# Optimization experiments

Measured on AMD Instinct MI355X. Metric: run time of the kernel, lower is better.

Reference implementation:

```python
import jax, jax.numpy as jnp
import numpy as np

B, L, T, F, H, O = 4096, 50, 64, 3, 20, 16

def setup_inputs() -> dict:
    key = jax.random.key(0)
    ks = jax.random.split(key, 20)
    p = lambda k, s: jax.random.normal(k, s, jnp.float32) * 0.1
    inp = {
        'x': jax.random.normal(ks[0], (B, L, T, F), jnp.float32),
        'lengths': jax.random.randint(ks[1], (B, L), 0, T, jnp.int32),
        # LSTMCell params (torch gate order i,f,g,o)
        'w_ih': p(ks[2], (4 * H, F)), 'w_hh': p(ks[3], (4 * H, H)),
        'b_ih': p(ks[4], (4 * H,)), 'b_hh': p(ks[5], (4 * H,)),
        # layer-summary Linear(20,16)
        'w_lin': p(ks[6], (O, H)), 'b_lin': p(ks[7], (O,)),
        # ClassifyNet convs
        'c1_w': p(ks[8], (32, 16, 5)), 'c1_b': p(ks[9], (32,)),
        'c2_w': p(ks[10], (32, 32, 4)), 'c2_b': p(ks[11], (32,)),
        'c3_w': p(ks[12], (32, 32, 4)), 'c3_b': p(ks[13], (32,)),
        'fc1_w': p(ks[14], (16, 32 * 19)), 'fc1_b': p(ks[15], (16,)),
        'fc2_w': p(ks[16], (4, 16)), 'fc2_b': p(ks[17], (4,)),
    }
    return inp

def _conv1d(x, w, b, stride):
    y = jax.lax.conv_general_dilated(x, w, (stride,), 'VALID',
                                     dimension_numbers=('NCH', 'OIH', 'NCH'))
    return y + b[None, :, None]

def _lstm_last_h(xseq, lens, w_ih, w_hh, b_ih, b_hh):
    # xseq: [N,T,F] padded; lens: [N]. Masked batched LSTM, returns h at step len-1.
    N = xseq.shape[0]
    xT = jnp.swapaxes(xseq, 0, 1)  # [T,N,F]
    h0 = jnp.zeros((N, H), xseq.dtype)
    def step(carry, inp):
        h, c = carry
        x_t, t = inp
        gates = x_t @ w_ih.T + b_ih + h @ w_hh.T + b_hh
        i, f, g, o = jnp.split(gates, 4, axis=-1)
        c_new = jax.nn.sigmoid(f) * c + jax.nn.sigmoid(i) * jnp.tanh(g)
        h_new = jax.nn.sigmoid(o) * jnp.tanh(c_new)
        m = (t < lens)[:, None]
        return (jnp.where(m, h_new, h), jnp.where(m, c_new, c)), None
    (h, _), _ = jax.lax.scan(step, (h0, h0), (xT, jnp.arange(xT.shape[0])))
    return h

def reference(x, lengths, w_ih, w_hh, b_ih, b_hh, w_lin, b_lin,
              c1_w, c1_b, c2_w, c2_b, c3_w, c3_b, fc1_w, fc1_b, fc2_w, fc2_b):
    N = B * L
    xf = x.reshape(N, T, F)
    lens = lengths.reshape(N)
    h = _lstm_last_h(xf, lens, w_ih, w_hh, b_ih, b_hh)          # [N,20]
    summ = jax.nn.sigmoid(h @ w_lin.T + b_lin)                   # [N,16]
    summ = jnp.where((lens > 0)[:, None], summ, 0.0)             # empty layer -> zeros
    feat = jnp.swapaxes(summ.reshape(B, L, O), 1, 2)             # [B,16,50]
    y = jax.nn.relu(_conv1d(feat, c1_w, c1_b, 1))                # [B,32,46]
    y = jax.nn.relu(_conv1d(y, c2_w, c2_b, 2))                   # [B,32,22]
    y = jax.nn.relu(_conv1d(y, c3_w, c3_b, 1))                   # [B,32,19]
    y = y.reshape(B, 32 * 19)
    y = jax.nn.relu(y @ fc1_w.T + fc1_b)
    return y @ fc2_w.T + fc2_b                                   # [B,4]
```

## Files before the change

kernel.cpp:

```cpp
#include <hip/hip_runtime.h>
#include <cstdint>
#include <cstddef>

#define NB 4096
#define NL 50
#define NT 64
#define NF 3
#define NH 20
#define NO 16
#define NN (NB*NL)
#define SB 16
#define WPB 2
#define TS 16
#define HSTR 20
#define XSTR 8
#define SCH (NN/64)

typedef __attribute__((ext_vector_type(8))) short bf16x8;
typedef __attribute__((ext_vector_type(4))) float f32x4;
typedef uint2 u2a __attribute__((may_alias));
typedef uint4 u4a __attribute__((may_alias));

#if defined(__has_builtin)
#  if __has_builtin(__builtin_amdgcn_exp2f)
#    define EXP2(x) __builtin_amdgcn_exp2f(x)
#  endif
#endif
#ifndef EXP2
extern "C" __device__ float __ocml_exp2_f32(float);
#  define EXP2(x) __ocml_exp2_f32(x)
#endif

__device__ __forceinline__ float fsig(float z) {
    return __builtin_amdgcn_rcpf(1.0f + __expf(-z));
}
__device__ __forceinline__ unsigned short f2bf(float f) {
    unsigned int x = __float_as_uint(f);
    x = (x + 0x7fffu + ((x >> 16) & 1u)) >> 16;
    return (unsigned short)x;
}
__device__ __forceinline__ float bf2f(unsigned short u) {
    return __uint_as_float(((unsigned int)u) << 16);
}
__device__ __forceinline__ unsigned int cvtpk(float a, float b) {
    unsigned int r;
    asm("v_cvt_pk_bf16_f32 %0, %1, %2" : "=v"(r) : "v"(a), "v"(b));
    return r;
}

__global__ __launch_bounds__(256) void hist64_kernel(const int* __restrict__ lengths,
                                                     int* __restrict__ bhist) {
    __shared__ int lh[64];
    const int tid = threadIdx.x;
    const int b   = blockIdx.x;
    if (tid < 64) lh[tid] = 0;
    __syncthreads();
    const int base = b * SCH;
    for (int i = tid; i < SCH; i += 256) {
        int len = lengths[base + i];
        len = len < 0 ? 0 : (len > 63 ? 63 : len);
        atomicAdd(&lh[len], 1);
    }
    __syncthreads();
    if (tid < 64) bhist[b * 64 + tid] = lh[tid];
}

__global__ __launch_bounds__(128) void prep_kernel(
    const int*   __restrict__ bhist,
    int*         __restrict__ boff,
    const float* __restrict__ w_hh,
    const float* __restrict__ b_ih,
    const float* __restrict__ b_hh,
    const float* __restrict__ w_ih,
    unsigned int* __restrict__ wfrag)
{
    int tid = threadIdx.x;
    if (tid < 64) {
        int l = tid;
        int tot = 0;
#pragma unroll 8
        for (int b = 0; b < 64; ++b) tot += bhist[b * 64 + l];
        int s = tot;
#pragma unroll
        for (int d = 1; d < 64; d <<= 1) {
            int o = __shfl_up(s, d);
            if (l >= d) s += o;
        }
        int run = s - tot;
#pragma unroll 8
        for (int b = 0; b < 64; ++b) {
            boff[b * 64 + l] = run;
            run += bhist[b * 64 + l];
        }
    } else {
        int l = tid - 64;
        int m = l & 15, kg = l >> 4;
        for (int T = 0; T < 5; ++T) {
            int g = (m & 3) * 20 + T * 4 + (m >> 2);
            int jt = g / 20;
            float sc = (jt == 2) ? 2.8853900817779268f : -1.4426950408889634f;
            unsigned int hi[4], lo[4];
            for (int d = 0; d < 4; ++d) {
                unsigned int hw[2], lw[2];
                for (int e = 0; e < 2; ++e) {
                    int k = kg * 8 + d * 2 + e;
                    float v = 0.0f;
                    if (k < 20)       v = w_hh[g * 20 + k];
                    else if (k <= 22) v = w_ih[g * 3 + (k - 20)];
                    else if (k == 23) v = b_ih[g] + b_hh[g];
                    else if (k <= 26) v = w_ih[g * 3 + (k - 24)];
                    v *= sc;
                    unsigned short h16 = f2bf(v);
                    float r = v - bf2f(h16);
                    hw[e] = h16; lw[e] = f2bf(r);
                }
                hi[d] = hw[0] | (hw[1] << 16);
                lo[d] = lw[0] | (lw[1] << 16);
            }
            for (int d = 0; d < 4; ++d) {
                wfrag[(size_t)((T * 2 + 0) * 64 + l) * 4 + d] = hi[d];
                wfrag[(size_t)((T * 2 + 1) * 64 + l) * 4 + d] = lo[d];
            }
        }
    }
}

__global__ __launch_bounds__(256) void scatter64_kernel(
    const int* __restrict__ lengths,
    const int* __restrict__ boff,
    int* __restrict__ order,
    int* __restrict__ len_s)
{
    __shared__ int lcnt[64];
    __shared__ int lbase[64];
    const int tid = threadIdx.x;
    const int b   = blockIdx.x;
    if (tid < 64) { lcnt[tid] = 0; lbase[tid] = boff[b * 64 + tid]; }
    __syncthreads();
    const int base = b * SCH;
    for (int i = tid; i < SCH; i += 256) {
        int n = base + i;
        int len = lengths[n];
        len = len < 0 ? 0 : (len > 63 ? 63 : len);
        int r = atomicAdd(&lcnt[len], 1);
        int pos = lbase[len] + r;
        order[pos] = n;
        len_s[pos] = len;
    }
}

#define LSTM_STEP(K, MASKED)                                                     \
    {                                                                            \
        uint2 ra_ = *(const u2a*)(p1 + (K) * st1);                               \
        uint2 rb_ = *(const u2a*)(p2 + (K) * st2);                               \
        union { uint4 u; bf16x8 v; } bb_;                                        \
        bb_.u = make_uint4(ra_.x, ra_.y, rb_.x, rb_.y);                          \
        f32x4 acc[5];                                                            \
        _Pragma("unroll")                                                        \
        for (int T = 0; T < 5; ++T) {                                            \
            f32x4 z4 = {0.f, 0.f, 0.f, 0.f};                                     \
            z4     = __builtin_amdgcn_mfma_f32_16x16x32_bf16(wf[2*T],   bb_.v, z4, 0, 0, 0); \
            acc[T] = __builtin_amdgcn_mfma_f32_16x16x32_bf16(wf[2*T+1], bb_.v, z4, 0, 0, 0); \
        }                                                                        \
        bool m_ = true;                                                          \
        if (MASKED) m_ = (t0 + (K)) < mylen;                                     \
        _Pragma("unroll")                                                        \
        for (int T = 0; T < 5; ++T) {                                            \
            float Ei = EXP2(acc[T][0]);                            \
            float Ef = EXP2(acc[T][1]);                            \
            float G  = EXP2(acc[T][2]);                           \
            float Eo = EXP2(acc[T][3]);                            \
            float Ai = 1.0f + Ei, Af = 1.0f + Ef, Bg = 1.0f + G;                 \
            float t1 = Ai * Bg;                                                  \
            float num = fmaf(G - 1.0f, Af, c5[T] * t1);                          \
            float cn  = num * __builtin_amdgcn_rcpf(t1 * Af);                    \
            float ce2 = fminf(cn * 2.8853900817779268f, 43.3f);                  \
            float Ec  = EXP2(ce2);                         \
            float hn  = (Ec - 1.0f) *                                            \
                        __builtin_amdgcn_rcpf((1.0f + Eo) * (1.0f + Ec));        \
        unsigned int hp_ = cvtpk(hn, hn);                                        \
        if (m_) {                                                                \
            c5[T] = cn;                                                          \
            hbf[wid][hoff + T * 4] = (unsigned short)hp_;                        \
        }                                                                        \
        }                                                                        \
    }

__global__ __launch_bounds__(128) void lstm_kernel(
    const float* __restrict__ x,
    const int*   __restrict__ len_s,
    const int*   __restrict__ order,
    const unsigned int* __restrict__ wfrag,
    const float* __restrict__ w_lin,
    const float* __restrict__ b_lin,
    float* __restrict__ feat)
{
    __shared__ __align__(16) unsigned short hbf[WPB][SB * HSTR];
    __shared__ __align__(16) unsigned short xbf[WPB][TS * SB * XSTR];
    __shared__ __align__(16) unsigned short zbuf[WPB][8];

    const int tid  = threadIdx.x;
    const int wid  = __builtin_amdgcn_readfirstlane(tid >> 6);
    const int lane = tid & 63;
    const int n16  = lane & 15;
    const int kg   = lane >> 4;
    const int base = ((gridDim.x - 1 - blockIdx.x) * WPB + wid) * SB;

    const int mylen   = len_s[base + n16];
    const int wavemin = len_s[base];
    const int wavemax = len_s[base + SB - 1];

    for (int i = lane; i < SB * HSTR; i += 64) hbf[wid][i] = 0;
    if (lane < 8) zbuf[wid][lane] = 0;

    bf16x8 wf[10];
#pragma unroll
    for (int p = 0; p < 10; ++p) {
        union { uint4 i; bf16x8 v; } cv;
        cv.i = ((const uint4*)wfrag)[p * 64 + lane];
        wf[p] = cv.v;
    }

    int nown = order[base + n16];
    const int ssl = lane >> 2;
    const int tq  = lane & 3;
    int nsl = __shfl(nown, ssl);
    const size_t gbase = (size_t)nsl * (NT * NF) + (size_t)tq * 12;

    const unsigned short* hpw = &hbf[wid][n16 * HSTR];
    const unsigned short* p1 = (kg < 3) ? (hpw + kg * 8)
                                        : &xbf[wid][n16 * XSTR + 4];
    const unsigned short* p2 = (kg < 2) ? (hpw + kg * 8 + 4)
                             : (kg == 2 ? &xbf[wid][n16 * XSTR]
                                        : &zbuf[wid][0]);
    const int st1 = (kg == 3) ? SB * XSTR : 0;
    const int st2 = (kg == 2) ? SB * XSTR : 0;
    const int hoff = n16 * HSTR + kg;

    float c5[5];
#pragma unroll
    for (int j = 0; j < 5; ++j) c5[j] = 0.0f;

    if (wavemax > 0) {
        float4 vf[3];
#pragma unroll
        for (int j = 0; j < 3; ++j) vf[j] = *(const float4*)(x + gbase + 4 * j);

        for (int t0 = 0; t0 < wavemax; t0 += TS) {
            float f12[12] = {vf[0].x, vf[0].y, vf[0].z, vf[0].w,
                             vf[1].x, vf[1].y, vf[1].z, vf[1].w,
                             vf[2].x, vf[2].y, vf[2].z, vf[2].w};
#pragma unroll
            for (int jj = 0; jj < 4; ++jj) {
                float a0 = f12[3 * jj], a1 = f12[3 * jj + 1], a2 = f12[3 * jj + 2];
                unsigned int w0 = cvtpk(a0, a1);
                unsigned int w1 = cvtpk(a2, 1.0f);
                float r0 = a0 - __uint_as_float(w0 << 16);
                float r1 = a1 - __uint_as_float(w0 & 0xFFFF0000u);
                float r2 = a2 - __uint_as_float(w1 << 16);
                unsigned int w2 = cvtpk(r0, r1);
                unsigned int w3 = cvtpk(r2, 0.0f);
                int t = tq * 4 + jj;
                *(u4a*)&xbf[wid][(t * SB + ssl) * XSTR] = make_uint4(w0, w1, w2, w3);
            }
            if (t0 + TS < wavemax) {
                size_t off = (size_t)(t0 + TS) * NF;
#pragma unroll
                for (int j = 0; j < 3; ++j)
                    vf[j] = *(const float4*)(x + gbase + off + 4 * j);
            }

            int kmax = wavemax - t0; if (kmax > TS) kmax = TS;
            int ku = wavemin - t0;
            ku = ku < 0 ? 0 : (ku > kmax ? kmax : ku);
            int k = 0;
            for (; k < ku; ++k)   LSTM_STEP(k, false)
            for (; k < kmax; ++k) LSTM_STEP(k, true)
        }
    }

    float hl[NH];
#pragma unroll
    for (int u = 0; u < NH; ++u) hl[u] = bf2f(hbf[wid][n16 * HSTR + u]);
    float4 res;
    if (mylen > 0) {
        float r4[4];
#pragma unroll
        for (int j = 0; j < 4; ++j) {
            int o = 4 * kg + j;
            float aa = b_lin[o];
#pragma unroll
            for (int kk = 0; kk < NH; ++kk) aa += w_lin[o * NH + kk] * hl[kk];
            r4[j] = fsig(aa);
        }
        res = make_float4(r4[0], r4[1], r4[2], r4[3]);
    } else {
        res = make_float4(0.f, 0.f, 0.f, 0.f);
    }
    *(float4*)(feat + (size_t)nown * NO + 4 * kg) = res;
}

__global__ __launch_bounds__(256) void head_kernel(
    const float* __restrict__ feat,
    const float* __restrict__ c1w, const float* __restrict__ c1b,
    const float* __restrict__ c2w, const float* __restrict__ c2b,
    const float* __restrict__ c3w, const float* __restrict__ c3b,
    const float* __restrict__ f1w, const float* __restrict__ f1b,
    const float* __restrict__ f2w, const float* __restrict__ f2b,
    float* __restrict__ out)
{
    const int b0  = blockIdx.x * 2;
    const int tid = threadIdx.x;
    const int p   = tid & 63;
    const int q   = __builtin_amdgcn_readfirstlane(tid >> 6);
    const int half = p >> 5;
    const int pp   = p & 31;

    __shared__ float sf[2][16 * 50];
    __shared__ float y1[2][32 * 46];
    __shared__ float y2[2][32 * 22];
    __shared__ __align__(16) float y3[2][32 * 19];
    __shared__ float r1[2][16];

    for (int i = tid; i < 2 * NL * NO; i += 256) {
        int bb = (i >= NL * NO) ? 1 : 0;
        int j = i - bb * (NL * NO);
        int l = j >> 4, o = j & 15;
        sf[bb][o * 50 + l] = feat[(size_t)(b0 + bb) * (NL * NO) + j];
    }
    __syncthreads();

    const int oc0 = q * 8;

#pragma unroll
    for (int bb = 0; bb < 2; ++bb) {
        if (p < 46) {
            float acc[8];
#pragma unroll
            for (int oc = 0; oc < 8; ++oc) acc[oc] = c1b[oc0 + oc];
#pragma unroll
            for (int ic = 0; ic < 16; ++ic) {
#pragma unroll
                for (int tap = 0; tap < 5; ++tap) {
                    float fv = sf[bb][ic * 50 + p + tap];
#pragma unroll
                    for (int oc = 0; oc < 8; ++oc)
                        acc[oc] += c1w[((oc0 + oc) * 16 + ic) * 5 + tap] * fv;
                }
            }
#pragma unroll
            for (int oc = 0; oc < 8; ++oc)
                y1[bb][(oc0 + oc) * 46 + p] = fmaxf(acc[oc], 0.0f);
        }
    }
    __syncthreads();

    if (pp < 22) {
        float acc[8];
#pragma unroll
        for (int oc = 0; oc < 8; ++oc) acc[oc] = c2b[oc0 + oc];
#pragma unroll
        for (int ic = 0; ic < 32; ++ic) {
#pragma unroll
            for (int tap = 0; tap < 4; ++tap) {
                float fv = y1[half][ic * 46 + 2 * pp + tap];
#pragma unroll
                for (int oc = 0; oc < 8; ++oc)
                    acc[oc] += c2w[((oc0 + oc) * 32 + ic) * 4 + tap] * fv;
            }
        }
#pragma unroll
        for (int oc = 0; oc < 8; ++oc)
            y2[half][(oc0 + oc) * 22 + pp] = fmaxf(acc[oc], 0.0f);
    }
    __syncthreads();

    if (pp < 19) {
        float acc[8];
#pragma unroll
        for (int oc = 0; oc < 8; ++oc) acc[oc] = c3b[oc0 + oc];
#pragma unroll
        for (int ic = 0; ic < 32; ++ic) {
#pragma unroll
            for (int tap = 0; tap < 4; ++tap) {
                float fv = y2[half][ic * 22 + pp + tap];
#pragma unroll
                for (int oc = 0; oc < 8; ++oc)
                    acc[oc] += c3w[((oc0 + oc) * 32 + ic) * 4 + tap] * fv;
            }
        }
#pragma unroll
        for (int oc = 0; oc < 8; ++oc)
            y3[half][(oc0 + oc) * 19 + pp] = fmaxf(acc[oc], 0.0f);
    }
    __syncthreads();

    if (q < 2) {
        int u  = p & 15;
        int qq = p >> 4;
        const float4* wv = (const float4*)(f1w + u * 608 + qq * 152);
        const float4* yv = (const float4*)(&y3[q][qq * 152]);
        float acc = 0.0f;
#pragma unroll 2
        for (int k = 0; k < 38; ++k) {
            float4 a = wv[k], bv = yv[k];
            acc += a.x * bv.x + a.y * bv.y + a.z * bv.z + a.w * bv.w;
        }
        acc += __shfl_xor(acc, 16);
        acc += __shfl_xor(acc, 32);
        if (p < 16) r1[q][p] = fmaxf(acc + f1b[p], 0.0f);
    }
    __syncthreads();

    if (q < 2 && p < 4) {
        float s = f2b[p];
#pragma unroll
        for (int k = 0; k < 16; ++k) s += f2w[p * 16 + k] * r1[q][k];
        out[(size_t)(b0 + q) * 4 + p] = s;
    }
}

extern "C" void kernel_launch(void* const* d_in, const int* in_sizes, int n_in,
                              void* d_out, int out_size, void* d_ws, size_t ws_size,
                              hipStream_t stream)
{
    const float* x     = (const float*)d_in[0];
    const int*  lengths= (const int*)  d_in[1];
    const float* w_ih  = (const float*)d_in[2];
    const float* w_hh  = (const float*)d_in[3];
    const float* b_ih  = (const float*)d_in[4];
    const float* b_hh  = (const float*)d_in[5];
    const float* w_lin = (const float*)d_in[6];
    const float* b_lin = (const float*)d_in[7];
    const float* c1w   = (const float*)d_in[8];
    const float* c1b   = (const float*)d_in[9];
    const float* c2w   = (const float*)d_in[10];
    const float* c2b   = (const float*)d_in[11];
    const float* c3w   = (const float*)d_in[12];
    const float* c3b   = (const float*)d_in[13];
    const float* f1w   = (const float*)d_in[14];
    const float* f1b   = (const float*)d_in[15];
    const float* f2w   = (const float*)d_in[16];
    const float* f2b   = (const float*)d_in[17];
    float* out = (float*)d_out;

    char* ws      = (char*)d_ws;
    float* feat   = (float*)ws;
    int*   order  = (int*)(feat + (size_t)NN * NO);
    int*   len_s  = order + NN;
    int*   bhist  = len_s + NN;
    int*   boff   = bhist + 64 * 64;
    unsigned int* wfrag = (unsigned int*)(boff + 64 * 64);

    hist64_kernel  <<<64, 256, 0, stream>>>(lengths, bhist);
    prep_kernel    <<<1, 128, 0, stream>>>(bhist, boff, w_hh, b_ih, b_hh, w_ih, wfrag);
    scatter64_kernel<<<64, 256, 0, stream>>>(lengths, boff, order, len_s);
    lstm_kernel    <<<NN / (SB * WPB), 128, 0, stream>>>(x, len_s, order, wfrag,
                                                         w_lin, b_lin, feat);
    head_kernel    <<<NB / 2, 256, 0, stream>>>(feat, c1w, c1b, c2w, c2b, c3w, c3b,
                                                f1w, f1b, f2w, f2b, out);
}
```

Before: 434.3 us.

## Batch LSTM reciprocals with product trick and fold prep kernel into hist/scatter

The LSTM step now shares one reciprocal across the five gate tiles for the cell update and one for the hidden output, using prefix and suffix products. This replaces ten rcp instructions per step with two plus extra multiplies. The tanh clamp is tightened from 43.3 to 14.5 so the product of five terms stays within float range. Separately, the single-block prep kernel is removed: weight fragment packing moves into an extra block of the histogram kernel, and each scatter block computes its own prefix offsets. This saves one launch and a serialized single-block stage.

```diff
diff --git a/kernel.cpp b/kernel.cpp
--- a/kernel.cpp
+++ b/kernel.cpp
@@ -48,11 +48,56 @@
     return r;
 }
 
-__global__ __launch_bounds__(256) void hist64_kernel(const int* __restrict__ lengths,
-                                                     int* __restrict__ bhist) {
+__device__ void wfrag_body(int l,
+                           const float* __restrict__ w_hh,
+                           const float* __restrict__ b_ih,
+                           const float* __restrict__ b_hh,
+                           const float* __restrict__ w_ih,
+                           unsigned int* __restrict__ wfrag)
+{
+    int m = l & 15, kg = l >> 4;
+    for (int T = 0; T < 5; ++T) {
+        int g = (m & 3) * 20 + T * 4 + (m >> 2);
+        int jt = g / 20;
+        float sc = (jt == 2) ? 2.8853900817779268f : -1.4426950408889634f;
+        unsigned int hi[4], lo[4];
+        for (int d = 0; d < 4; ++d) {
+            unsigned int hw[2], lw[2];
+            for (int e = 0; e < 2; ++e) {
+                int k = kg * 8 + d * 2 + e;
+                float v = 0.0f;
+                if (k < 20)       v = w_hh[g * 20 + k];
+                else if (k <= 22) v = w_ih[g * 3 + (k - 20)];
+                else if (k == 23) v = b_ih[g] + b_hh[g];
+                else if (k <= 26) v = w_ih[g * 3 + (k - 24)];
+                v *= sc;
+                unsigned short h16 = f2bf(v);
+                float r = v - bf2f(h16);
+                hw[e] = h16; lw[e] = f2bf(r);
+            }
+            hi[d] = hw[0] | (hw[1] << 16);
+            lo[d] = lw[0] | (lw[1] << 16);
+        }
+        for (int d = 0; d < 4; ++d) {
+            wfrag[(size_t)((T * 2 + 0) * 64 + l) * 4 + d] = hi[d];
+            wfrag[(size_t)((T * 2 + 1) * 64 + l) * 4 + d] = lo[d];
+        }
+    }
+}
+
+__global__ __launch_bounds__(256) void hist64_kernel(
+    const int* __restrict__ lengths, int* __restrict__ bhist,
+    const float* __restrict__ w_hh, const float* __restrict__ b_ih,
+    const float* __restrict__ b_hh, const float* __restrict__ w_ih,
+    unsigned int* __restrict__ wfrag)
+{
+    const int b = blockIdx.x;
+    const int tid = threadIdx.x;
+    if (b == 64) {
+        if (tid < 64) wfrag_body(tid, w_hh, b_ih, b_hh, w_ih, wfrag);
+        return;
+    }
     __shared__ int lh[64];
-    const int tid = threadIdx.x;
-    const int b   = blockIdx.x;
     if (tid < 64) lh[tid] = 0;
     __syncthreads();
     const int base = b * SCH;
@@ -65,69 +110,9 @@
     if (tid < 64) bhist[b * 64 + tid] = lh[tid];
 }
 
-__global__ __launch_bounds__(128) void prep_kernel(
-    const int*   __restrict__ bhist,
-    int*         __restrict__ boff,
-    const float* __restrict__ w_hh,
-    const float* __restrict__ b_ih,
-    const float* __restrict__ b_hh,
-    const float* __restrict__ w_ih,
-    unsigned int* __restrict__ wfrag)
-{
-    int tid = threadIdx.x;
-    if (tid < 64) {
-        int l = tid;
-        int tot = 0;
-#pragma unroll 8
-        for (int b = 0; b < 64; ++b) tot += bhist[b * 64 + l];
-        int s = tot;
-#pragma unroll
-        for (int d = 1; d < 64; d <<= 1) {
-            int o = __shfl_up(s, d);
-            if (l >= d) s += o;
-        }
-        int run = s - tot;
-#pragma unroll 8
-        for (int b = 0; b < 64; ++b) {
-            boff[b * 64 + l] = run;
-            run += bhist[b * 64 + l];
-        }
-    } else {
-        int l = tid - 64;
-        int m = l & 15, kg = l >> 4;
-        for (int T = 0; T < 5; ++T) {
-            int g = (m & 3) * 20 + T * 4 + (m >> 2);
-            int jt = g / 20;
-            float sc = (jt == 2) ? 2.8853900817779268f : -1.4426950408889634f;
-            unsigned int hi[4], lo[4];
-            for (int d = 0; d < 4; ++d) {
-                unsigned int hw[2], lw[2];
-                for (int e = 0; e < 2; ++e) {
-                    int k = kg * 8 + d * 2 + e;
-                    float v = 0.0f;
-                    if (k < 20)       v = w_hh[g * 20 + k];
-                    else if (k <= 22) v = w_ih[g * 3 + (k - 20)];
-                    else if (k == 23) v = b_ih[g] + b_hh[g];
-                    else if (k <= 26) v = w_ih[g * 3 + (k - 24)];
-                    v *= sc;
-                    unsigned short h16 = f2bf(v);
-                    float r = v - bf2f(h16);
-                    hw[e] = h16; lw[e] = f2bf(r);
-                }
-                hi[d] = hw[0] | (hw[1] << 16);
-                lo[d] = lw[0] | (lw[1] << 16);
-            }
-            for (int d = 0; d < 4; ++d) {
-                wfrag[(size_t)((T * 2 + 0) * 64 + l) * 4 + d] = hi[d];
-                wfrag[(size_t)((T * 2 + 1) * 64 + l) * 4 + d] = lo[d];
-            }
-        }
-    }
-}
-
 __global__ __launch_bounds__(256) void scatter64_kernel(
     const int* __restrict__ lengths,
-    const int* __restrict__ boff,
+    const int* __restrict__ bhist,
     int* __restrict__ order,
     int* __restrict__ len_s)
 {
@@ -135,7 +120,24 @@
     __shared__ int lbase[64];
     const int tid = threadIdx.x;
     const int b   = blockIdx.x;
-    if (tid < 64) { lcnt[tid] = 0; lbase[tid] = boff[b * 64 + tid]; }
+    if (tid < 64) {
+        const int l = tid;
+        int tot = 0, pre = 0;
+#pragma unroll 16
+        for (int bb = 0; bb < 64; ++bb) {
+            int v = bhist[bb * 64 + l];
+            tot += v;
+            if (bb < b) pre += v;
+        }
+        int s = tot;
+#pragma unroll
+        for (int d = 1; d < 64; d <<= 1) {
+            int o = __shfl_up(s, d);
+            if (l >= d) s += o;
+        }
+        lbase[l] = (s - tot) + pre;
+        lcnt[l] = 0;
+    }
     __syncthreads();
     const int base = b * SCH;
     for (int i = tid; i < SCH; i += 256) {
@@ -164,25 +166,54 @@
         }                                                                        \
         bool m_ = true;                                                          \
         if (MASKED) m_ = (t0 + (K)) < mylen;                                     \
+        float num_[5], dd_[5], ao_[5];                                           \
         _Pragma("unroll")                                                        \
         for (int T = 0; T < 5; ++T) {                                            \
             float Ei = EXP2(acc[T][0]);                            \
             float Ef = EXP2(acc[T][1]);                            \
             float G  = EXP2(acc[T][2]);                           \
-            float Eo = EXP2(acc[T][3]);                            \
             float Ai = 1.0f + Ei, Af = 1.0f + Ef, Bg = 1.0f + G;                 \
             float t1 = Ai * Bg;                                                  \
-            float num = fmaf(G - 1.0f, Af, c5[T] * t1);                          \
-            float cn  = num * __builtin_amdgcn_rcpf(t1 * Af);                    \
-            float ce2 = fminf(cn * 2.8853900817779268f, 43.3f);                  \
+            num_[T] = fmaf(G - 1.0f, Af, c5[T] * t1);                            \
+            dd_[T]  = t1 * Af;                                                   \
+            ao_[T]  = acc[T][3];                                                 \
+        }                                                                        \
+        float s0_ = dd_[0], s1_ = s0_ * dd_[1], s2_ = s1_ * dd_[2];              \
+        float s3_ = s2_ * dd_[3], P_ = s3_ * dd_[4];                             \
+        float u3_ = dd_[3] * dd_[4], u2_ = dd_[2] * u3_, u1_ = dd_[1] * u2_;     \
+        float R_ = __builtin_amdgcn_rcpf(P_);                                    \
+        float cn_[5];                                                            \
+        cn_[0] = num_[0] * (R_ * u1_);                                           \
+        cn_[1] = num_[1] * (R_ * s0_ * u2_);                                     \
+        cn_[2] = num_[2] * (R_ * s1_ * u3_);                                     \
+        cn_[3] = num_[3] * (R_ * s2_ * dd_[4]);                                  \
+        cn_[4] = num_[4] * (R_ * s3_);                                           \
+        float em_[5], e2_[5];                                                    \
+        _Pragma("unroll")                                                        \
+        for (int T = 0; T < 5; ++T) {                                            \
+            float ce2 = fminf(cn_[T] * 2.8853900817779268f, 14.5f);              \
             float Ec  = EXP2(ce2);                         \
-            float hn  = (Ec - 1.0f) *                                            \
-                        __builtin_amdgcn_rcpf((1.0f + Eo) * (1.0f + Ec));        \
-        unsigned int hp_ = cvtpk(hn, hn);                                        \
-        if (m_) {                                                                \
-            c5[T] = cn;                                                          \
-            hbf[wid][hoff + T * 4] = (unsigned short)hp_;                        \
+            float Eo  = EXP2(ao_[T]);                              \
+            em_[T] = Ec - 1.0f;                                                  \
+            e2_[T] = (1.0f + Eo) * (1.0f + Ec);                                  \
         }                                                                        \
+        float q0_ = e2_[0], q1_ = q0_ * e2_[1], q2_ = q1_ * e2_[2];              \
+        float q3_ = q2_ * e2_[3], Q_ = q3_ * e2_[4];                             \
+        float v3_ = e2_[3] * e2_[4], v2_ = e2_[2] * v3_, v1_ = e2_[1] * v2_;     \
+        float R2_ = __builtin_amdgcn_rcpf(Q_);                                   \
+        float hn_[5];                                                            \
+        hn_[0] = em_[0] * (R2_ * v1_);                                           \
+        hn_[1] = em_[1] * (R2_ * q0_ * v2_);                                     \
+        hn_[2] = em_[2] * (R2_ * q1_ * v3_);                                     \
+        hn_[3] = em_[3] * (R2_ * q2_ * e2_[4]);                                  \
+        hn_[4] = em_[4] * (R2_ * q3_);                                           \
+        _Pragma("unroll")                                                        \
+        for (int T = 0; T < 5; ++T) {                                            \
+            unsigned int hp_ = cvtpk(hn_[T], hn_[T]);                            \
+            if (m_) {                                                            \
+                c5[T] = cn_[T];                                                  \
+                hbf[wid][hoff + T * 4] = (unsigned short)hp_;                    \
+            }                                                                    \
         }                                                                        \
     }
 
@@ -449,14 +480,13 @@
     int*   order  = (int*)(feat + (size_t)NN * NO);
     int*   len_s  = order + NN;
     int*   bhist  = len_s + NN;
-    int*   boff   = bhist + 64 * 64;
-    unsigned int* wfrag = (unsigned int*)(boff + 64 * 64);
-
-    hist64_kernel  <<<64, 256, 0, stream>>>(lengths, bhist);
-    prep_kernel    <<<1, 128, 0, stream>>>(bhist, boff, w_hh, b_ih, b_hh, w_ih, wfrag);
-    scatter64_kernel<<<64, 256, 0, stream>>>(lengths, boff, order, len_s);
-    lstm_kernel    <<<NN / (SB * WPB), 128, 0, stream>>>(x, len_s, order, wfrag,
-                                                         w_lin, b_lin, feat);
-    head_kernel    <<<NB / 2, 256, 0, stream>>>(feat, c1w, c1b, c2w, c2b, c3w, c3b,
-                                                f1w, f1b, f2w, f2b, out);
-}
+    unsigned int* wfrag = (unsigned int*)(bhist + 64 * 64);
+
+    hist64_kernel   <<<65, 256, 0, stream>>>(lengths, bhist,
+                                             w_hh, b_ih, b_hh, w_ih, wfrag);
+    scatter64_kernel<<<64, 256, 0, stream>>>(lengths, bhist, order, len_s);
+    lstm_kernel     <<<NN / (SB * WPB), 128, 0, stream>>>(x, len_s, order, wfrag,
+                                                          w_lin, b_lin, feat);
+    head_kernel     <<<NB / 2, 256, 0, stream>>>(feat, c1w, c1b, c2w, c2b, c3w, c3b,
+                                                 f1w, f1b, f2w, f2b, out);
+}
```

Measured after the change: 449.2 us. +3.4%, slower.

## Fuse histogram, prefix and scatter into one kernel with a grid-wide flag barrier

Applied to the files above, without the earlier changes.

Merges the three counting-sort launches (hist, prep, scatter) into a single kernel. The 64 blocks publish their histograms and then spin on per-block magic flags until all are visible, and a 65th block builds the weight fragments. The head kernel resets the flags for the next call. In the LSTM kernel the weight-fragment loads move inside the wavemax>0 branch, so all-empty waves skip them. This cuts two kernel launches and their gaps, but relies on all 65 blocks being co-resident for the spin barrier.

```diff
diff --git a/kernel.cpp b/kernel.cpp
--- a/kernel.cpp
+++ b/kernel.cpp
@@ -15,6 +15,7 @@
 #define HSTR 20
 #define XSTR 8
 #define SCH (NN/64)
+#define FLAGV(b) (0x9E3779B9u + (unsigned)(b) * 0x85EBCA6Bu)
 
 typedef __attribute__((ext_vector_type(8))) short bf16x8;
 typedef __attribute__((ext_vector_type(4))) float f32x4;
@@ -48,11 +49,62 @@
     return r;
 }
 
-__global__ __launch_bounds__(256) void hist64_kernel(const int* __restrict__ lengths,
-                                                     int* __restrict__ bhist) {
+__device__ void wfrag_body(int l,
+                           const float* __restrict__ w_hh,
+                           const float* __restrict__ b_ih,
+                           const float* __restrict__ b_hh,
+                           const float* __restrict__ w_ih,
+                           unsigned int* __restrict__ wfrag)
+{
+    int m = l & 15, kg = l >> 4;
+    for (int T = 0; T < 5; ++T) {
+        int g = (m & 3) * 20 + T * 4 + (m >> 2);
+        int jt = g / 20;
+        float sc = (jt == 2) ? 2.8853900817779268f : -1.4426950408889634f;
+        unsigned int hi[4], lo[4];
+        for (int d = 0; d < 4; ++d) {
+            unsigned int hw[2], lw[2];
+            for (int e = 0; e < 2; ++e) {
+                int k = kg * 8 + d * 2 + e;
+                float v = 0.0f;
+                if (k < 20)       v = w_hh[g * 20 + k];
+                else if (k <= 22) v = w_ih[g * 3 + (k - 20)];
+                else if (k == 23) v = b_ih[g] + b_hh[g];
+                else if (k <= 26) v = w_ih[g * 3 + (k - 24)];
+                v *= sc;
+                unsigned short h16 = f2bf(v);
+                float r = v - bf2f(h16);
+                hw[e] = h16; lw[e] = f2bf(r);
+            }
+            hi[d] = hw[0] | (hw[1] << 16);
+            lo[d] = lw[0] | (lw[1] << 16);
+        }
+        for (int d = 0; d < 4; ++d) {
+            wfrag[(size_t)((T * 2 + 0) * 64 + l) * 4 + d] = hi[d];
+            wfrag[(size_t)((T * 2 + 1) * 64 + l) * 4 + d] = lo[d];
+        }
+    }
+}
+
+__global__ __launch_bounds__(256) void sort_kernel(
+    const int* __restrict__ lengths,
+    int* __restrict__ bhist,
+    unsigned int* __restrict__ flags,
+    int* __restrict__ order,
+    int* __restrict__ len_s,
+    const float* __restrict__ w_hh, const float* __restrict__ b_ih,
+    const float* __restrict__ b_hh, const float* __restrict__ w_ih,
+    unsigned int* __restrict__ wfrag)
+{
+    const int b   = blockIdx.x;
+    const int tid = threadIdx.x;
+    if (b == 64) {
+        if (tid < 64) wfrag_body(tid, w_hh, b_ih, b_hh, w_ih, wfrag);
+        return;
+    }
     __shared__ int lh[64];
-    const int tid = threadIdx.x;
-    const int b   = blockIdx.x;
+    __shared__ int lcnt[64];
+    __shared__ int lbase[64];
     if (tid < 64) lh[tid] = 0;
     __syncthreads();
     const int base = b * SCH;
@@ -63,81 +115,40 @@
     }
     __syncthreads();
     if (tid < 64) bhist[b * 64 + tid] = lh[tid];
-}
-
-__global__ __launch_bounds__(128) void prep_kernel(
-    const int*   __restrict__ bhist,
-    int*         __restrict__ boff,
-    const float* __restrict__ w_hh,
-    const float* __restrict__ b_ih,
-    const float* __restrict__ b_hh,
-    const float* __restrict__ w_ih,
-    unsigned int* __restrict__ wfrag)
-{
-    int tid = threadIdx.x;
+    __syncthreads();
+    if (tid == 0) {
+        __threadfence();
+        __hip_atomic_store(&flags[b], FLAGV(b), __ATOMIC_RELEASE,
+                           __HIP_MEMORY_SCOPE_AGENT);
+    }
     if (tid < 64) {
-        int l = tid;
-        int tot = 0;
-#pragma unroll 8
-        for (int b = 0; b < 64; ++b) tot += bhist[b * 64 + l];
+        while (__hip_atomic_load(&flags[tid], __ATOMIC_ACQUIRE,
+                                 __HIP_MEMORY_SCOPE_AGENT) != FLAGV(tid)) {
+            __builtin_amdgcn_s_sleep(8);
+        }
+    }
+    __syncthreads();
+    __threadfence();
+
+    if (tid < 64) {
+        const int l = tid;
+        int tot = 0, pre = 0;
+#pragma unroll 16
+        for (int bb = 0; bb < 64; ++bb) {
+            int v = bhist[bb * 64 + l];
+            tot += v;
+            if (bb < b) pre += v;
+        }
         int s = tot;
 #pragma unroll
         for (int d = 1; d < 64; d <<= 1) {
             int o = __shfl_up(s, d);
             if (l >= d) s += o;
         }
-        int run = s - tot;
-#pragma unroll 8
-        for (int b = 0; b < 64; ++b) {
-            boff[b * 64 + l] = run;
-            run += bhist[b * 64 + l];
-        }
-    } else {
-        int l = tid - 64;
-        int m = l & 15, kg = l >> 4;
-        for (int T = 0; T < 5; ++T) {
-            int g = (m & 3) * 20 + T * 4 + (m >> 2);
-            int jt = g / 20;
-            float sc = (jt == 2) ? 2.8853900817779268f : -1.4426950408889634f;
-            unsigned int hi[4], lo[4];
-            for (int d = 0; d < 4; ++d) {
-                unsigned int hw[2], lw[2];
-                for (int e = 0; e < 2; ++e) {
-                    int k = kg * 8 + d * 2 + e;
-                    float v = 0.0f;
-                    if (k < 20)       v = w_hh[g * 20 + k];
-                    else if (k <= 22) v = w_ih[g * 3 + (k - 20)];
-                    else if (k == 23) v = b_ih[g] + b_hh[g];
-                    else if (k <= 26) v = w_ih[g * 3 + (k - 24)];
-                    v *= sc;
-                    unsigned short h16 = f2bf(v);
-                    float r = v - bf2f(h16);
-                    hw[e] = h16; lw[e] = f2bf(r);
-                }
-                hi[d] = hw[0] | (hw[1] << 16);
-                lo[d] = lw[0] | (lw[1] << 16);
-            }
-            for (int d = 0; d < 4; ++d) {
-                wfrag[(size_t)((T * 2 + 0) * 64 + l) * 4 + d] = hi[d];
-                wfrag[(size_t)((T * 2 + 1) * 64 + l) * 4 + d] = lo[d];
-            }
-        }
-    }
-}
-
-__global__ __launch_bounds__(256) void scatter64_kernel(
-    const int* __restrict__ lengths,
-    const int* __restrict__ boff,
-    int* __restrict__ order,
-    int* __restrict__ len_s)
-{
-    __shared__ int lcnt[64];
-    __shared__ int lbase[64];
-    const int tid = threadIdx.x;
-    const int b   = blockIdx.x;
-    if (tid < 64) { lcnt[tid] = 0; lbase[tid] = boff[b * 64 + tid]; }
-    __syncthreads();
-    const int base = b * SCH;
+        lbase[l] = (s - tot) + pre;
+        lcnt[l] = 0;
+    }
+    __syncthreads();
     for (int i = tid; i < SCH; i += 256) {
         int n = base + i;
         int len = lengths[n];
@@ -213,14 +224,6 @@
     for (int i = lane; i < SB * HSTR; i += 64) hbf[wid][i] = 0;
     if (lane < 8) zbuf[wid][lane] = 0;
 
-    bf16x8 wf[10];
-#pragma unroll
-    for (int p = 0; p < 10; ++p) {
-        union { uint4 i; bf16x8 v; } cv;
-        cv.i = ((const uint4*)wfrag)[p * 64 + lane];
-        wf[p] = cv.v;
-    }
-
     int nown = order[base + n16];
     const int ssl = lane >> 2;
     const int tq  = lane & 3;
@@ -242,6 +245,14 @@
     for (int j = 0; j < 5; ++j) c5[j] = 0.0f;
 
     if (wavemax > 0) {
+        bf16x8 wf[10];
+#pragma unroll
+        for (int p = 0; p < 10; ++p) {
+            union { uint4 i; bf16x8 v; } cv;
+            cv.i = ((const uint4*)wfrag)[p * 64 + lane];
+            wf[p] = cv.v;
+        }
+
         float4 vf[3];
 #pragma unroll
         for (int j = 0; j < 3; ++j) vf[j] = *(const float4*)(x + gbase + 4 * j);
@@ -302,6 +313,7 @@
 
 __global__ __launch_bounds__(256) void head_kernel(
     const float* __restrict__ feat,
+    unsigned int* __restrict__ flags,
     const float* __restrict__ c1w, const float* __restrict__ c1b,
     const float* __restrict__ c2w, const float* __restrict__ c2b,
     const float* __restrict__ c3w, const float* __restrict__ c3b,
@@ -315,6 +327,8 @@
     const int q   = __builtin_amdgcn_readfirstlane(tid >> 6);
     const int half = p >> 5;
     const int pp   = p & 31;
+
+    if (blockIdx.x == 0 && tid < 64) flags[tid] = 0u;
 
     __shared__ float sf[2][16 * 50];
     __shared__ float y1[2][32 * 46];
@@ -449,14 +463,14 @@
     int*   order  = (int*)(feat + (size_t)NN * NO);
     int*   len_s  = order + NN;
     int*   bhist  = len_s + NN;
-    int*   boff   = bhist + 64 * 64;
-    unsigned int* wfrag = (unsigned int*)(boff + 64 * 64);
-
-    hist64_kernel  <<<64, 256, 0, stream>>>(lengths, bhist);
-    prep_kernel    <<<1, 128, 0, stream>>>(bhist, boff, w_hh, b_ih, b_hh, w_ih, wfrag);
-    scatter64_kernel<<<64, 256, 0, stream>>>(lengths, boff, order, len_s);
-    lstm_kernel    <<<NN / (SB * WPB), 128, 0, stream>>>(x, len_s, order, wfrag,
-                                                         w_lin, b_lin, feat);
-    head_kernel    <<<NB / 2, 256, 0, stream>>>(feat, c1w, c1b, c2w, c2b, c3w, c3b,
-                                                f1w, f1b, f2w, f2b, out);
-}
+    unsigned int* flags = (unsigned int*)(bhist + 64 * 64);
+    unsigned int* wfrag = flags + 64;
+
+    sort_kernel <<<65, 256, 0, stream>>>(lengths, bhist, flags, order, len_s,
+                                         w_hh, b_ih, b_hh, w_ih, wfrag);
+    lstm_kernel <<<NN / (SB * WPB), 128, 0, stream>>>(x, len_s, order, wfrag,
+                                                      w_lin, b_lin, feat);
+    head_kernel <<<NB / 2, 256, 0, stream>>>(feat, flags,
+                                             c1w, c1b, c2w, c2b, c3w, c3b,
+                                             f1w, f1b, f2w, f2b, out);
+}
```

Result: no change. 431.4 us (-0.7%).
